# Performance work log

Hardware: AMD Instinct MI355X
Metric: run time of the kernel (lower is better)

Reference implementation:

```python
import jax, jax.numpy as jnp
import numpy as np

B = 4096      # batch
N = 32768     # total tree nodes (real + pseudo classes) = columns of x
L = 12        # tree path depth (levels)
K = 64        # siblings (brother nodes) per level, padded to fixed width
C = 16384     # number of real classes (range of y)


def setup_inputs() -> dict:
    key = jax.random.key(0)
    k1, k2, k3, k4 = jax.random.split(key, 4)
    x = jax.random.normal(k1, (B, N), dtype=jnp.float32)
    # per-level sibling index sets (constants derived from the cover tree /
    # new2index / index2brother dicts in the original module)
    brother = jax.random.randint(k2, (L, K), 0, N)
    # the true path node at each level must be one of that level's siblings
    pos = jax.random.randint(k3, (L,), 0, K)
    p_y = brother[jnp.arange(L), pos]
    y = jax.random.randint(k4, (B,), 0, C)  # class labels (path selection baked into brother/p_y)
    return {"x": x, "brother": brother, "p_y": p_y, "y": y}


def reference(x, brother, p_y, y):
    # x: [B, N] logits over all tree nodes; brother: [L, K]; p_y: [L]
    gathered = x[:, brother]                      # [B, L, K] irregular column gather
    logp = jax.nn.log_softmax(gathered, axis=-1)  # per-level softmax over siblings
    # label = first position of the path node within its sibling set (torch nonzero()[0])
    labels = jnp.argmax(brother == p_y[:, None], axis=-1)          # [L]
    sel = jnp.take_along_axis(logp, labels[None, :, None], axis=2)[..., 0]  # [B, L]
    # CrossEntropyLoss = mean over batch of NLL, summed across tree levels
    return (-sel).mean(axis=0).sum()
```

## Files before the change

kernel.cpp:

```cpp
#include <hip/hip_runtime.h>

#define BB 4096
#define NN 32768
#define LL 12
#define KK 64

constexpr int CHUNK = 8;
constexpr int NWAVES = LL * (BB / CHUNK);
constexpr int WPB = 4;
constexpr int NBLOCKS = NWAVES / WPB;

__global__ __launch_bounds__(256) void hsm_partial(
    const float* __restrict__ x,
    const int* __restrict__ brother,
    const int* __restrict__ p_y,
    float* __restrict__ partials) {

    const int wave_in_block = threadIdx.x >> 6;
    const int lane = threadIdx.x & 63;
    const int wid = blockIdx.x * WPB + wave_in_block;

    const int chunk = wid / LL;
    const int l = wid - chunk * LL;
    const int b0 = chunk * CHUNK;

    const int col = brother[l * KK + lane];
    const int py = p_y[l];
    const int label = __ffsll(__ballot(col == py)) - 1;

    const float* __restrict__ xp = x + (size_t)b0 * NN + col;

    float v[CHUNK];
    #pragma unroll
    for (int bi = 0; bi < CHUNK; ++bi)
        v[bi] = xp[(size_t)bi * NN];

    float local = 0.f;
    #pragma unroll
    for (int bi = 0; bi < CHUNK; ++bi) {
        float mx = v[bi];
        #pragma unroll
        for (int o = 32; o > 0; o >>= 1) mx = fmaxf(mx, __shfl_xor(mx, o));
        float s = __expf(v[bi] - mx);
        #pragma unroll
        for (int o = 32; o > 0; o >>= 1) s += __shfl_xor(s, o);
        const float lse = mx + __logf(s);
        local += lse - __shfl(v[bi], label);
    }

    __shared__ float red[WPB];
    if (lane == 0) red[wave_in_block] = local;
    __syncthreads();
    if (threadIdx.x == 0) {
        float s = 0.f;
        #pragma unroll
        for (int i = 0; i < WPB; ++i) s += red[i];
        partials[blockIdx.x] = s;
    }
}

__global__ __launch_bounds__(256) void hsm_final(
    const float* __restrict__ partials, float* __restrict__ out, int n) {
    float s = 0.f;
    for (int i = threadIdx.x; i < n; i += 256) s += partials[i];
    #pragma unroll
    for (int o = 32; o > 0; o >>= 1) s += __shfl_xor(s, o);
    __shared__ float red[4];
    const int wave = threadIdx.x >> 6, lane = threadIdx.x & 63;
    if (lane == 0) red[wave] = s;
    __syncthreads();
    if (threadIdx.x == 0) {
        out[0] = (red[0] + red[1] + red[2] + red[3]) / (float)BB;
    }
}

extern "C" void kernel_launch(void* const* d_in, const int* in_sizes, int n_in,
                              void* d_out, int out_size, void* d_ws, size_t ws_size,
                              hipStream_t stream) {
    const float* x       = (const float*)d_in[0];
    const int*   brother = (const int*)d_in[1];
    const int*   p_y     = (const int*)d_in[2];
    float* out      = (float*)d_out;
    float* partials = (float*)d_ws;

    hsm_partial<<<NBLOCKS, 256, 0, stream>>>(x, brother, p_y, partials);
    hsm_final<<<1, 256, 0, stream>>>(partials, out, NBLOCKS);
}
```

Before: 636.6 us.

## Stream full rows into LDS and gather sibling columns into compact buffer

Adds a pre-pass kernel in which each block copies one whole row of x into LDS with coalesced float4 loads. It then gathers the 768 sibling columns into a compact workspace G. The softmax kernel then reads contiguous G instead of scattered columns of x. This replaces many uncoalesced, cache-line-wasting gathers with a full sequential read of x, at the cost of reading all 512MB of x and using 128KB of LDS per block, which limits occupancy.

```diff
diff --git a/kernel.cpp b/kernel.cpp
--- a/kernel.cpp
+++ b/kernel.cpp
@@ -4,6 +4,24 @@
 #define NN 32768
 #define LL 12
 #define KK 64
+#define SLOTS (LL * KK)
+
+
+__global__ __launch_bounds__(1024) void extract_rows(
+    const float* __restrict__ x,
+    const int* __restrict__ brother,
+    float* __restrict__ G) {
+    __shared__ float row[NN];
+    const int b = blockIdx.x;
+    const float4* __restrict__ src = (const float4*)(x + (size_t)b * NN);
+    float4* dst = (float4*)row;
+    #pragma unroll
+    for (int i = 0; i < NN / 4 / 1024; ++i)
+        dst[threadIdx.x + i * 1024] = src[threadIdx.x + i * 1024];
+    __syncthreads();
+    if (threadIdx.x < SLOTS)
+        G[(size_t)b * SLOTS + threadIdx.x] = row[brother[threadIdx.x]];
+}
 
 constexpr int CHUNK = 8;
 constexpr int NWAVES = LL * (BB / CHUNK);
@@ -11,7 +29,7 @@
 constexpr int NBLOCKS = NWAVES / WPB;
 
 __global__ __launch_bounds__(256) void hsm_partial(
-    const float* __restrict__ x,
+    const float* __restrict__ G,
     const int* __restrict__ brother,
     const int* __restrict__ p_y,
     float* __restrict__ partials) {
@@ -19,21 +37,19 @@
     const int wave_in_block = threadIdx.x >> 6;
     const int lane = threadIdx.x & 63;
     const int wid = blockIdx.x * WPB + wave_in_block;
-
     const int chunk = wid / LL;
     const int l = wid - chunk * LL;
     const int b0 = chunk * CHUNK;
 
     const int col = brother[l * KK + lane];
-    const int py = p_y[l];
-    const int label = __ffsll(__ballot(col == py)) - 1;
+    const int label = __ffsll(__ballot(col == p_y[l])) - 1;
 
-    const float* __restrict__ xp = x + (size_t)b0 * NN + col;
+    const float* __restrict__ gp = G + (size_t)b0 * SLOTS + l * KK + lane;
 
     float v[CHUNK];
     #pragma unroll
     for (int bi = 0; bi < CHUNK; ++bi)
-        v[bi] = xp[(size_t)bi * NN];
+        v[bi] = gp[(size_t)bi * SLOTS];
 
     float local = 0.f;
     #pragma unroll
@@ -44,8 +60,7 @@
         float s = __expf(v[bi] - mx);
         #pragma unroll
         for (int o = 32; o > 0; o >>= 1) s += __shfl_xor(s, o);
-        const float lse = mx + __logf(s);
-        local += lse - __shfl(v[bi], label);
+        local += mx + __logf(s) - __shfl(v[bi], label);
     }
 
     __shared__ float red[WPB];
@@ -80,9 +95,12 @@
     const float* x       = (const float*)d_in[0];
     const int*   brother = (const int*)d_in[1];
     const int*   p_y     = (const int*)d_in[2];
-    float* out      = (float*)d_out;
-    float* partials = (float*)d_ws;
+    float* out = (float*)d_out;
 
-    hsm_partial<<<NBLOCKS, 256, 0, stream>>>(x, brother, p_y, partials);
+    float* G        = (float*)d_ws;
+    float* partials = G + (size_t)BB * SLOTS;
+
+    extract_rows<<<BB, 1024, 0, stream>>>(x, brother, G);
+    hsm_partial<<<NBLOCKS, 256, 0, stream>>>(G, brother, p_y, partials);
     hsm_final<<<1, 256, 0, stream>>>(partials, out, NBLOCKS);
 }
```

Result: slower. 680.5 us (+6.9%).

## Process all levels per wave and replace final reduction kernel with atomics

Applied to the files above, without the earlier changes.

Each wave now handles all 12 tree levels for 4 batch rows instead of one level for 8 rows. Index and label setup is hoisted per wave, and the loads within each row are more concentrated. The separate final reduction kernel is replaced by a tiny zeroing kernel plus per-block float atomicAdd into the output. This trades a second reduction pass for atomic contention on one address and non-deterministic summation order. Higher register use from v[12][4] may lower occupancy.

```diff
diff --git a/kernel.cpp b/kernel.cpp
--- a/kernel.cpp
+++ b/kernel.cpp
@@ -5,47 +5,57 @@
 #define LL 12
 #define KK 64
 
-constexpr int CHUNK = 8;
-constexpr int NWAVES = LL * (BB / CHUNK);
+constexpr int CHUNK = 4;
+constexpr int NWAVES = BB / CHUNK;
 constexpr int WPB = 4;
 constexpr int NBLOCKS = NWAVES / WPB;
 
-__global__ __launch_bounds__(256) void hsm_partial(
+__global__ __launch_bounds__(64) void zero_out(float* out, int n) {
+    if ((int)threadIdx.x < n) out[threadIdx.x] = 0.f;
+}
+
+__global__ __launch_bounds__(256) void hsm_fused(
     const float* __restrict__ x,
     const int* __restrict__ brother,
     const int* __restrict__ p_y,
-    float* __restrict__ partials) {
+    float* __restrict__ out) {
 
     const int wave_in_block = threadIdx.x >> 6;
     const int lane = threadIdx.x & 63;
     const int wid = blockIdx.x * WPB + wave_in_block;
+    const int b0 = wid * CHUNK;
 
-    const int chunk = wid / LL;
-    const int l = wid - chunk * LL;
-    const int b0 = chunk * CHUNK;
+    int col[LL];
+    int label[LL];
+    #pragma unroll
+    for (int l = 0; l < LL; ++l) {
+        col[l] = brother[l * KK + lane];
+        label[l] = __ffsll(__ballot(col[l] == p_y[l])) - 1;
+    }
 
-    const int col = brother[l * KK + lane];
-    const int py = p_y[l];
-    const int label = __ffsll(__ballot(col == py)) - 1;
-
-    const float* __restrict__ xp = x + (size_t)b0 * NN + col;
-
-    float v[CHUNK];
+    float v[LL][CHUNK];
     #pragma unroll
-    for (int bi = 0; bi < CHUNK; ++bi)
-        v[bi] = xp[(size_t)bi * NN];
+    for (int c = 0; c < CHUNK; ++c) {
+        const float* __restrict__ xr = x + (size_t)(b0 + c) * NN;
+        #pragma unroll
+        for (int l = 0; l < LL; ++l)
+            v[l][c] = xr[col[l]];
+    }
 
     float local = 0.f;
     #pragma unroll
-    for (int bi = 0; bi < CHUNK; ++bi) {
-        float mx = v[bi];
+    for (int l = 0; l < LL; ++l) {
         #pragma unroll
-        for (int o = 32; o > 0; o >>= 1) mx = fmaxf(mx, __shfl_xor(mx, o));
-        float s = __expf(v[bi] - mx);
-        #pragma unroll
-        for (int o = 32; o > 0; o >>= 1) s += __shfl_xor(s, o);
-        const float lse = mx + __logf(s);
-        local += lse - __shfl(v[bi], label);
+        for (int c = 0; c < CHUNK; ++c) {
+            const float val = v[l][c];
+            float mx = val;
+            #pragma unroll
+            for (int o = 32; o > 0; o >>= 1) mx = fmaxf(mx, __shfl_xor(mx, o));
+            float s = __expf(val - mx);
+            #pragma unroll
+            for (int o = 32; o > 0; o >>= 1) s += __shfl_xor(s, o);
+            local += mx + __logf(s) - __shfl(val, label[l]);
+        }
     }
 
     __shared__ float red[WPB];
@@ -55,22 +65,7 @@
         float s = 0.f;
         #pragma unroll
         for (int i = 0; i < WPB; ++i) s += red[i];
-        partials[blockIdx.x] = s;
-    }
-}
-
-__global__ __launch_bounds__(256) void hsm_final(
-    const float* __restrict__ partials, float* __restrict__ out, int n) {
-    float s = 0.f;
-    for (int i = threadIdx.x; i < n; i += 256) s += partials[i];
-    #pragma unroll
-    for (int o = 32; o > 0; o >>= 1) s += __shfl_xor(s, o);
-    __shared__ float red[4];
-    const int wave = threadIdx.x >> 6, lane = threadIdx.x & 63;
-    if (lane == 0) red[wave] = s;
-    __syncthreads();
-    if (threadIdx.x == 0) {
-        out[0] = (red[0] + red[1] + red[2] + red[3]) / (float)BB;
+        atomicAdd(out, s * (1.0f / (float)BB));
     }
 }
 
@@ -80,9 +75,8 @@
     const float* x       = (const float*)d_in[0];
     const int*   brother = (const int*)d_in[1];
     const int*   p_y     = (const int*)d_in[2];
-    float* out      = (float*)d_out;
-    float* partials = (float*)d_ws;
+    float* out = (float*)d_out;
 
-    hsm_partial<<<NBLOCKS, 256, 0, stream>>>(x, brother, p_y, partials);
-    hsm_final<<<1, 256, 0, stream>>>(partials, out, NBLOCKS);
+    zero_out<<<1, 64, 0, stream>>>(out, out_size);
+    hsm_fused<<<NBLOCKS, 256, 0, stream>>>(x, brother, p_y, out);
 }
```

Result: no change. 645.7 us (+1.4%).
